# Performance work log

Measured on AMD Instinct MI355X. Metric: run time of the kernel, lower is better.

The kernel has to match this reference:

```python
import jax, jax.numpy as jnp
import numpy as np


def setup_inputs() -> dict:
    key = jax.random.key(0)
    x = jax.random.normal(key, (8192, 8192), dtype=jnp.float32)
    return {"x": x, "k": 64}


def reference(x, k):
    # k-th largest value per row: equivalent to sort-descending[..., k-1],
    # but computed with an O(n) partial selection instead of a full sort.
    topv = jax.lax.top_k(x, k)[0]          # [B, k]
    kth = topv[..., -1:]                   # [B, 1] k-th largest
    return x * (x >= kth).astype(x.dtype)  # keep values >= k-th largest
```

## Files before the change

### kernel.cpp

```cpp
#include <hip/hip_runtime.h>
#include <stdint.h>

#define NT 256
#define ROW 8192

__device__ __forceinline__ uint32_t f2u(uint32_t b) {
    return (b & 0x80000000u) ? ~b : (b | 0x80000000u);
}
__device__ __forceinline__ uint32_t u2fbits(uint32_t u) {
    return (u & 0x80000000u) ? (u ^ 0x80000000u) : ~u;
}

template <int B>
__device__ __forceinline__ void select_digit(const uint32_t* s_hist, uint32_t* s_wsum,
                                             uint32_t* s_sel, int t, uint32_t k) {
    uint32_t local = 0;
    if (B == 16) {
#pragma unroll
        for (int j = 0; j < 4; ++j) {
            uint4 h = ((const uint4*)s_hist)[t * 4 + j];
            local += h.x + h.y + h.z + h.w;
        }
    } else {
        uint4 h = ((const uint4*)s_hist)[t];
        local = h.x + h.y + h.z + h.w;
    }
    const int lane = t & 63;
    const int wave = t >> 6;
    uint32_t incl = local;
#pragma unroll
    for (int off = 1; off < 64; off <<= 1) {
        uint32_t vv = __shfl_down(incl, off, 64);
        if (lane + off < 64) incl += vv;
    }
    if (lane == 0) s_wsum[wave] = incl;
    __syncthreads();
    uint32_t later = 0;
#pragma unroll
    for (int w = 0; w < 4; ++w)
        if (w > wave) later += s_wsum[w];
    const uint32_t sfx_incl = incl + later;
    const uint32_t sfx_excl = sfx_incl - local;
    if (sfx_excl < k && k <= sfx_incl) {
        uint32_t cum = sfx_excl;
#pragma unroll
        for (int i = B - 1; i >= 0; --i) {
            uint32_t c = s_hist[t * B + i];
            if (k <= cum + c) {
                s_sel[0] = (uint32_t)(t * B + i);
                s_sel[1] = k - cum;
                break;
            }
            cum += c;
        }
    }
    __syncthreads();
}

__global__ __launch_bounds__(NT) void ksparse_rowtopk(const float* __restrict__ x,
                                                      const int* __restrict__ kp,
                                                      float* __restrict__ out) {
    __shared__ uint32_t s_hist[4096];
    __shared__ uint32_t s_wsum[4];
    __shared__ uint32_t s_sel[2];

    const int t = threadIdx.x;
    const long long rowbase = (long long)blockIdx.x * (long long)ROW;
    const uint4* xin = (const uint4*)(x + rowbase);

    uint4 v[8];
#pragma unroll
    for (int j = 0; j < 8; ++j) v[j] = xin[j * NT + t];
#pragma unroll
    for (int j = 0; j < 8; ++j) {
        v[j].x = f2u(v[j].x);
        v[j].y = f2u(v[j].y);
        v[j].z = f2u(v[j].z);
        v[j].w = f2u(v[j].w);
    }

    int kin = *kp;
    if (kin < 1) kin = 1;
    if (kin > ROW) kin = ROW;
    uint32_t k = (uint32_t)kin;

#pragma unroll
    for (int j = 0; j < 4; ++j)
        ((uint4*)s_hist)[j * NT + t] = make_uint4(0u, 0u, 0u, 0u);
    __syncthreads();
#pragma unroll
    for (int j = 0; j < 8; ++j) {
        atomicAdd(&s_hist[v[j].x >> 20], 1u);
        atomicAdd(&s_hist[v[j].y >> 20], 1u);
        atomicAdd(&s_hist[v[j].z >> 20], 1u);
        atomicAdd(&s_hist[v[j].w >> 20], 1u);
    }
    __syncthreads();
    select_digit<16>(s_hist, s_wsum, s_sel, t, k);
    uint32_t d1 = s_sel[0];
    k = s_sel[1];
    __syncthreads();

    ((uint4*)s_hist)[t] = make_uint4(0u, 0u, 0u, 0u);
    __syncthreads();
#pragma unroll
    for (int j = 0; j < 8; ++j) {
        if ((v[j].x >> 20) == d1) atomicAdd(&s_hist[(v[j].x >> 10) & 1023u], 1u);
        if ((v[j].y >> 20) == d1) atomicAdd(&s_hist[(v[j].y >> 10) & 1023u], 1u);
        if ((v[j].z >> 20) == d1) atomicAdd(&s_hist[(v[j].z >> 10) & 1023u], 1u);
        if ((v[j].w >> 20) == d1) atomicAdd(&s_hist[(v[j].w >> 10) & 1023u], 1u);
    }
    __syncthreads();
    select_digit<4>(s_hist, s_wsum, s_sel, t, k);
    uint32_t d2 = s_sel[0];
    k = s_sel[1];
    __syncthreads();

    const uint32_t pfx2 = (d1 << 10) | d2;
    ((uint4*)s_hist)[t] = make_uint4(0u, 0u, 0u, 0u);
    __syncthreads();
#pragma unroll
    for (int j = 0; j < 8; ++j) {
        if ((v[j].x >> 10) == pfx2) atomicAdd(&s_hist[v[j].x & 1023u], 1u);
        if ((v[j].y >> 10) == pfx2) atomicAdd(&s_hist[v[j].y & 1023u], 1u);
        if ((v[j].z >> 10) == pfx2) atomicAdd(&s_hist[v[j].z & 1023u], 1u);
        if ((v[j].w >> 10) == pfx2) atomicAdd(&s_hist[v[j].w & 1023u], 1u);
    }
    __syncthreads();
    select_digit<4>(s_hist, s_wsum, s_sel, t, k);
    uint32_t d3 = s_sel[0];

    const uint32_t thr = (d1 << 20) | (d2 << 10) | d3;

    float4* orow = (float4*)(out + rowbase);
#pragma unroll
    for (int j = 0; j < 8; ++j) {
        float4 o;
        o.x = (v[j].x >= thr) ? __uint_as_float(u2fbits(v[j].x)) : 0.0f;
        o.y = (v[j].y >= thr) ? __uint_as_float(u2fbits(v[j].y)) : 0.0f;
        o.z = (v[j].z >= thr) ? __uint_as_float(u2fbits(v[j].z)) : 0.0f;
        o.w = (v[j].w >= thr) ? __uint_as_float(u2fbits(v[j].w)) : 0.0f;
        orow[j * NT + t] = o;
    }
}

extern "C" void kernel_launch(void* const* d_in, const int* in_sizes, int n_in,
                              void* d_out, int out_size, void* d_ws, size_t ws_size,
                              hipStream_t stream) {
    const float* x = (const float*)d_in[0];
    const int* kp = (const int*)d_in[1];
    float* out = (float*)d_out;
    const int rows = in_sizes[0] / ROW;
    ksparse_rowtopk<<<dim3(rows), dim3(NT), 0, stream>>>(x, kp, out);
}
```

Before: 436.4 us.

## Sample-based pre-filter to skip most atomics in first radix histogram

```diff
diff --git a/kernel.cpp b/kernel.cpp
--- a/kernel.cpp
+++ b/kernel.cpp
@@ -57,6 +57,18 @@
     __syncthreads();
 }
 
+__device__ __forceinline__ uint32_t block_sum(uint32_t cnt, uint32_t* s_wsum, int t) {
+    const int lane = t & 63;
+    const int wave = t >> 6;
+#pragma unroll
+    for (int off = 32; off >= 1; off >>= 1) cnt += __shfl_down(cnt, off, 64);
+    if (lane == 0) s_wsum[wave] = cnt;
+    __syncthreads();
+    uint32_t tot = s_wsum[0] + s_wsum[1] + s_wsum[2] + s_wsum[3];
+    __syncthreads();
+    return tot;
+}
+
 __global__ __launch_bounds__(NT) void ksparse_rowtopk(const float* __restrict__ x,
                                                       const int* __restrict__ kp,
                                                       float* __restrict__ out) {
@@ -88,12 +100,40 @@
     for (int j = 0; j < 4; ++j)
         ((uint4*)s_hist)[j * NT + t] = make_uint4(0u, 0u, 0u, 0u);
     __syncthreads();
+    atomicAdd(&s_hist[v[0].x >> 20], 1u);
+    atomicAdd(&s_hist[v[2].x >> 20], 1u);
+    atomicAdd(&s_hist[v[4].x >> 20], 1u);
+    atomicAdd(&s_hist[v[6].x >> 20], 1u);
+    __syncthreads();
+    uint32_t starget = (3u * k + 7u) / 8u;
+    if (starget < 1u) starget = 1u;
+    if (starget > 1023u) starget = 1023u;
+    select_digit<16>(s_hist, s_wsum, s_sel, t, starget);
+    uint32_t selBin = s_sel[0];
+    __syncthreads();
+
+    uint32_t cnt = 0;
 #pragma unroll
     for (int j = 0; j < 8; ++j) {
-        atomicAdd(&s_hist[v[j].x >> 20], 1u);
-        atomicAdd(&s_hist[v[j].y >> 20], 1u);
-        atomicAdd(&s_hist[v[j].z >> 20], 1u);
-        atomicAdd(&s_hist[v[j].w >> 20], 1u);
+        cnt += (v[j].x >> 20) >= selBin;
+        cnt += (v[j].y >> 20) >= selBin;
+        cnt += (v[j].z >> 20) >= selBin;
+        cnt += (v[j].w >> 20) >= selBin;
+    }
+    uint32_t C = block_sum(cnt, s_wsum, t);
+    if (C < k) selBin = 0u;
+
+#pragma unroll
+    for (int j = 0; j < 4; ++j)
+        ((uint4*)s_hist)[j * NT + t] = make_uint4(0u, 0u, 0u, 0u);
+    __syncthreads();
+#pragma unroll
+    for (int j = 0; j < 8; ++j) {
+        uint32_t bx = v[j].x >> 20, by = v[j].y >> 20, bz = v[j].z >> 20, bw = v[j].w >> 20;
+        if (bx >= selBin) atomicAdd(&s_hist[bx], 1u);
+        if (by >= selBin) atomicAdd(&s_hist[by], 1u);
+        if (bz >= selBin) atomicAdd(&s_hist[bz], 1u);
+        if (bw >= selBin) atomicAdd(&s_hist[bw], 1u);
     }
     __syncthreads();
     select_digit<16>(s_hist, s_wsum, s_sel, t, k);
```

Result: no change. 438.6 us (+0.5%).

## Double threads per row, use two histogram buffers to drop barriers

Applied to the files above, without the earlier changes.

```diff
diff --git a/kernel.cpp b/kernel.cpp
--- a/kernel.cpp
+++ b/kernel.cpp
@@ -1,8 +1,9 @@
 #include <hip/hip_runtime.h>
 #include <stdint.h>
 
-#define NT 256
+#define NT 512
 #define ROW 8192
+#define VPT 4
 
 __device__ __forceinline__ uint32_t f2u(uint32_t b) {
     return (b & 0x80000000u) ? ~b : (b | 0x80000000u);
@@ -15,15 +16,13 @@
 __device__ __forceinline__ void select_digit(const uint32_t* s_hist, uint32_t* s_wsum,
                                              uint32_t* s_sel, int t, uint32_t k) {
     uint32_t local = 0;
-    if (B == 16) {
-#pragma unroll
-        for (int j = 0; j < 4; ++j) {
-            uint4 h = ((const uint4*)s_hist)[t * 4 + j];
-            local += h.x + h.y + h.z + h.w;
-        }
+    if (B == 8) {
+        uint4 h0 = ((const uint4*)s_hist)[t * 2];
+        uint4 h1 = ((const uint4*)s_hist)[t * 2 + 1];
+        local = h0.x + h0.y + h0.z + h0.w + h1.x + h1.y + h1.z + h1.w;
     } else {
-        uint4 h = ((const uint4*)s_hist)[t];
-        local = h.x + h.y + h.z + h.w;
+        uint2 h = ((const uint2*)s_hist)[t];
+        local = h.x + h.y;
     }
     const int lane = t & 63;
     const int wave = t >> 6;
@@ -37,7 +36,7 @@
     __syncthreads();
     uint32_t later = 0;
 #pragma unroll
-    for (int w = 0; w < 4; ++w)
+    for (int w = 0; w < 8; ++w)
         if (w > wave) later += s_wsum[w];
     const uint32_t sfx_incl = incl + later;
     const uint32_t sfx_excl = sfx_incl - local;
@@ -57,84 +56,78 @@
     __syncthreads();
 }
 
-__global__ __launch_bounds__(NT) void ksparse_rowtopk(const float* __restrict__ x,
-                                                      const int* __restrict__ kp,
-                                                      float* __restrict__ out) {
-    __shared__ uint32_t s_hist[4096];
-    __shared__ uint32_t s_wsum[4];
+__global__ __launch_bounds__(NT, 8) void ksparse_rowtopk(const float* __restrict__ x,
+                                                         const int* __restrict__ kp,
+                                                         float* __restrict__ out) {
+    __shared__ uint32_t s_hist1[4096];
+    __shared__ uint32_t s_hist2[1024];
+    __shared__ uint32_t s_wsum[8];
     __shared__ uint32_t s_sel[2];
 
     const int t = threadIdx.x;
     const long long rowbase = (long long)blockIdx.x * (long long)ROW;
     const uint4* xin = (const uint4*)(x + rowbase);
 
-    uint4 v[8];
+    uint4 v[VPT];
 #pragma unroll
-    for (int j = 0; j < 8; ++j) v[j] = xin[j * NT + t];
-#pragma unroll
-    for (int j = 0; j < 8; ++j) {
-        v[j].x = f2u(v[j].x);
-        v[j].y = f2u(v[j].y);
-        v[j].z = f2u(v[j].z);
-        v[j].w = f2u(v[j].w);
-    }
+    for (int j = 0; j < VPT; ++j) v[j] = xin[j * NT + t];
+
+    ((uint4*)s_hist1)[t] = make_uint4(0u, 0u, 0u, 0u);
+    ((uint4*)s_hist1)[t + NT] = make_uint4(0u, 0u, 0u, 0u);
+    if (t < 256) ((uint4*)s_hist2)[t] = make_uint4(0u, 0u, 0u, 0u);
 
     int kin = *kp;
     if (kin < 1) kin = 1;
     if (kin > ROW) kin = ROW;
     uint32_t k = (uint32_t)kin;
+    __syncthreads();
 
 #pragma unroll
-    for (int j = 0; j < 4; ++j)
-        ((uint4*)s_hist)[j * NT + t] = make_uint4(0u, 0u, 0u, 0u);
-    __syncthreads();
-#pragma unroll
-    for (int j = 0; j < 8; ++j) {
-        atomicAdd(&s_hist[v[j].x >> 20], 1u);
-        atomicAdd(&s_hist[v[j].y >> 20], 1u);
-        atomicAdd(&s_hist[v[j].z >> 20], 1u);
-        atomicAdd(&s_hist[v[j].w >> 20], 1u);
+    for (int j = 0; j < VPT; ++j) {
+        v[j].x = f2u(v[j].x);
+        v[j].y = f2u(v[j].y);
+        v[j].z = f2u(v[j].z);
+        v[j].w = f2u(v[j].w);
+        atomicAdd(&s_hist1[v[j].x >> 20], 1u);
+        atomicAdd(&s_hist1[v[j].y >> 20], 1u);
+        atomicAdd(&s_hist1[v[j].z >> 20], 1u);
+        atomicAdd(&s_hist1[v[j].w >> 20], 1u);
     }
     __syncthreads();
-    select_digit<16>(s_hist, s_wsum, s_sel, t, k);
-    uint32_t d1 = s_sel[0];
+    select_digit<8>(s_hist1, s_wsum, s_sel, t, k);
+    const uint32_t d1 = s_sel[0];
     k = s_sel[1];
-    __syncthreads();
 
-    ((uint4*)s_hist)[t] = make_uint4(0u, 0u, 0u, 0u);
-    __syncthreads();
+    if (t < 256) ((uint4*)s_hist1)[t] = make_uint4(0u, 0u, 0u, 0u);
 #pragma unroll
-    for (int j = 0; j < 8; ++j) {
-        if ((v[j].x >> 20) == d1) atomicAdd(&s_hist[(v[j].x >> 10) & 1023u], 1u);
-        if ((v[j].y >> 20) == d1) atomicAdd(&s_hist[(v[j].y >> 10) & 1023u], 1u);
-        if ((v[j].z >> 20) == d1) atomicAdd(&s_hist[(v[j].z >> 10) & 1023u], 1u);
-        if ((v[j].w >> 20) == d1) atomicAdd(&s_hist[(v[j].w >> 10) & 1023u], 1u);
+    for (int j = 0; j < VPT; ++j) {
+        if ((v[j].x >> 20) == d1) atomicAdd(&s_hist2[(v[j].x >> 10) & 1023u], 1u);
+        if ((v[j].y >> 20) == d1) atomicAdd(&s_hist2[(v[j].y >> 10) & 1023u], 1u);
+        if ((v[j].z >> 20) == d1) atomicAdd(&s_hist2[(v[j].z >> 10) & 1023u], 1u);
+        if ((v[j].w >> 20) == d1) atomicAdd(&s_hist2[(v[j].w >> 10) & 1023u], 1u);
     }
     __syncthreads();
-    select_digit<4>(s_hist, s_wsum, s_sel, t, k);
-    uint32_t d2 = s_sel[0];
+    select_digit<2>(s_hist2, s_wsum, s_sel, t, k);
+    const uint32_t d2 = s_sel[0];
     k = s_sel[1];
-    __syncthreads();
 
     const uint32_t pfx2 = (d1 << 10) | d2;
-    ((uint4*)s_hist)[t] = make_uint4(0u, 0u, 0u, 0u);
-    __syncthreads();
 #pragma unroll
-    for (int j = 0; j < 8; ++j) {
-        if ((v[j].x >> 10) == pfx2) atomicAdd(&s_hist[v[j].x & 1023u], 1u);
-        if ((v[j].y >> 10) == pfx2) atomicAdd(&s_hist[v[j].y & 1023u], 1u);
-        if ((v[j].z >> 10) == pfx2) atomicAdd(&s_hist[v[j].z & 1023u], 1u);
-        if ((v[j].w >> 10) == pfx2) atomicAdd(&s_hist[v[j].w & 1023u], 1u);
+    for (int j = 0; j < VPT; ++j) {
+        if ((v[j].x >> 10) == pfx2) atomicAdd(&s_hist1[v[j].x & 1023u], 1u);
+        if ((v[j].y >> 10) == pfx2) atomicAdd(&s_hist1[v[j].y & 1023u], 1u);
+        if ((v[j].z >> 10) == pfx2) atomicAdd(&s_hist1[v[j].z & 1023u], 1u);
+        if ((v[j].w >> 10) == pfx2) atomicAdd(&s_hist1[v[j].w & 1023u], 1u);
     }
     __syncthreads();
-    select_digit<4>(s_hist, s_wsum, s_sel, t, k);
-    uint32_t d3 = s_sel[0];
+    select_digit<2>(s_hist1, s_wsum, s_sel, t, k);
+    const uint32_t d3 = s_sel[0];
 
     const uint32_t thr = (d1 << 20) | (d2 << 10) | d3;
 
     float4* orow = (float4*)(out + rowbase);
 #pragma unroll
-    for (int j = 0; j < 8; ++j) {
+    for (int j = 0; j < VPT; ++j) {
         float4 o;
         o.x = (v[j].x >= thr) ? __uint_as_float(u2fbits(v[j].x)) : 0.0f;
         o.y = (v[j].y >= thr) ? __uint_as_float(u2fbits(v[j].y)) : 0.0f;
```

Measured after the change: 435.2 us. Within noise of the previous version (-0.3%).
